# Kernel optimization log

Measured on AMD Instinct MI355X. Metric: run time of the kernel, lower is better.

## Reference

```python
import jax, jax.numpy as jnp
import numpy as np

BN_EPS = 1e-3  # Keras BatchNormalization default epsilon


def lstm_layer(x, h0, c0, W, U, b):
    # x: [B,T,D]; Keras gate order: i, f, g(cell), o
    def step(carry, xt):
        h, c = carry
        z = xt @ W + h @ U + b               # [B,4H]
        i, f, g, o = jnp.split(z, 4, axis=-1)
        c = jax.nn.sigmoid(f) * c + jax.nn.sigmoid(i) * jnp.tanh(g)
        h = jax.nn.sigmoid(o) * jnp.tanh(c)
        return (h, c), h
    (h, c), ys = jax.lax.scan(step, (h0, c0), x.transpose(1, 0, 2))
    return ys.transpose(1, 0, 2), h, c       # [B,T,H], [B,H], [B,H]


def setup_inputs() -> dict:
    key = jax.random.key(0)
    ks = jax.random.split(key, 8)
    B, T, V, D, H = 64, 128, 32000, 256, 1024
    s = 0.05
    return {
        "tokens": jax.random.randint(ks[0], (B, T), 0, V, dtype=jnp.int32),
        "h0": jnp.zeros((B, H), jnp.float32),
        "c0": jnp.zeros((B, H), jnp.float32),
        "emb": jax.random.normal(ks[1], (V, D), jnp.float32) * s,
        "W0": jax.random.normal(ks[2], (D, 4 * H), jnp.float32) * s,
        "U0": jax.random.normal(ks[3], (H, 4 * H), jnp.float32) * s,
        "b0": jnp.zeros((4 * H,), jnp.float32),
        "W1": jax.random.normal(ks[4], (H, 4 * H), jnp.float32) * s,
        "U1": jax.random.normal(ks[5], (H, 4 * H), jnp.float32) * s,
        "b1": jnp.zeros((4 * H,), jnp.float32),
        "gamma": jnp.ones((H,), jnp.float32),
        "beta": jnp.zeros((H,), jnp.float32),
        "mov_mean": jnp.zeros((H,), jnp.float32),
        "mov_var": jnp.ones((H,), jnp.float32),
    }


def reference(tokens, h0, c0, emb, W0, U0, b0, W1, U1, b1, gamma, beta, mov_mean, mov_var):
    x = emb[tokens]                                   # [B,T,D] embedding lookup
    # Original call() feeds the SAME `hidden` as initial state of layer 0,
    # then the (h,c) of layer 0 as initial state of layer 1 — replicate that.
    x, h, c = lstm_layer(x, h0, c0, W0, U0, b0)
    out, h, c = lstm_layer(x, h, c, W1, U1, b1)
    # BatchNormalization at inference (dropout inactive, moving stats used)
    inv = jax.lax.rsqrt(mov_var + BN_EPS)
    norm = (out - mov_mean) * inv * gamma + beta
    return norm, h, c
```

## Files before the change

### kernel.cpp

```cpp
#include <hip/hip_runtime.h>
#include <hip/hip_bf16.h>


typedef __attribute__((ext_vector_type(8))) short short8;
typedef __attribute__((ext_vector_type(4))) short short4v;
typedef __attribute__((ext_vector_type(4))) float f32x4;
typedef __attribute__((ext_vector_type(16))) float f32x16;
typedef unsigned short ushort_t;

__device__ __forceinline__ void lgkm0_bar() {
  asm volatile("s_waitcnt lgkmcnt(0)" ::: "memory");
  __builtin_amdgcn_s_barrier();
}

__device__ __forceinline__ ushort_t f2b(float f) {
  __hip_bfloat16 h = __float2bfloat16(f);
  return *reinterpret_cast<ushort_t*>(&h);
}
__device__ __forceinline__ float b2f(ushort_t u) {
  unsigned int x = ((unsigned int)u) << 16;
  return __builtin_bit_cast(float, x);
}
__device__ __forceinline__ float fsigmoid(float x) {
  return 1.f / (1.f + __expf(-x));
}
__device__ __forceinline__ float ftanh(float x) {
  return 1.f - 2.f / (__expf(2.f * x) + 1.f);
}

__device__ __forceinline__ void gload_lds16(const ushort_t* g, ushort_t* l) {
  __builtin_amdgcn_global_load_lds(
      (const __attribute__((address_space(1))) unsigned int*)g,
      (__attribute__((address_space(3))) unsigned int*)l, 16, 0, 0);
}

__device__ __forceinline__ size_t chunkoff(int b, int kcg, int NKS) {
  return (size_t)((((b >> 5) * NKS + (kcg >> 1)) << 6) |
                  ((b & 31) | ((kcg & 1) << 5))) * 8;
}

__global__ __launch_bounds__(256) void k_convert(
    const float* __restrict__ src, ushort_t* __restrict__ dst, int kshift) {
  size_t tid = (size_t)blockIdx.x * 256 + threadIdx.x;
  int k = (int)(tid >> 12);
  int c = (int)(tid & 4095);
  int pc = ((c & 1023) << 2) | (c >> 10);
  dst[((size_t)pc << kshift) + k] = f2b(src[tid]);
}

__global__ __launch_bounds__(256) void k_convert_ucoop(
    const float* __restrict__ src, ushort_t* __restrict__ dst) {
  int cid = blockIdx.x * 256 + threadIdx.x;
  int l = cid & 63;
  int ks = (cid >> 6) & 63;
  int nt = (cid >> 12) & 1;
  int w = cid >> 13;
  int pc = w * 64 + nt * 32 + (l & 31);
  int c = ((pc & 3) << 10) | (pc >> 2);
  int kb = ks * 16 + (l >> 5) * 8;
  short8 v;
#pragma unroll
  for (int e = 0; e < 8; ++e)
    v[e] = (short)f2b(src[(size_t)(kb + e) * 4096 + c]);
  *(short8*)(dst + (size_t)cid * 8) = v;
}

__global__ __launch_bounds__(256) void k_bias(
    const float* __restrict__ b0, const float* __restrict__ b1,
    float* __restrict__ bp0, float* __restrict__ bp1) {
  int pc = blockIdx.x * 256 + threadIdx.x;
  int c = ((pc & 3) << 10) | (pc >> 2);
  bp0[pc] = b0[c];
  bp1[pc] = b1[c];
}

__global__ __launch_bounds__(256) void k_gather(
    const int* __restrict__ tokens, const float* __restrict__ emb,
    ushort_t* __restrict__ Xef) {
  int row = blockIdx.x;
  int t = row >> 6, b = row & 63;
  int tok = tokens[b * 128 + t];
  int d = threadIdx.x;
  Xef[(size_t)t * 16384 + chunkoff(b, d >> 3, 16) + (d & 7)] =
      f2b(emb[(size_t)tok * 256 + d]);
}

__global__ __launch_bounds__(256) void k_init(
    const float* __restrict__ h0, const float* __restrict__ c0,
    ushort_t* __restrict__ hall, float* __restrict__ c_st,
    unsigned* __restrict__ bars) {
  int tid = blockIdx.x * 256 + threadIdx.x;
  int b = tid >> 10, jj = tid & 1023;
  c_st[tid] = c0[tid];
  hall[chunkoff(b, jj >> 3, 64) + (jj & 7)] = f2b(h0[tid]);
  if (tid < 2) bars[tid] = 0;
}

template <int NKS>
__global__ __launch_bounds__(256) void k_gemm(
    const ushort_t* __restrict__ Af, const ushort_t* __restrict__ BT,
    ushort_t* __restrict__ C) {
  const int K = NKS * 16;
  const int xcd = blockIdx.x & 7, loc = blockIdx.x >> 3;
  const int wgM = xcd * 8 + (loc & 7);
  const int wgN = loc >> 3;
  const int tid = threadIdx.x;
  const int l = tid & 63;
  const int wv = tid >> 6;
  const int wvM = wv & 1, wvN = wv >> 1;

  __shared__ __align__(16) ushort_t Alds[4096];
  __shared__ __align__(16) ushort_t Blds[4096];

  const int m0 = wgM * 128, n0 = wgN * 128;
  f32x4 acc[4][4] = {};

  for (int k0 = 0; k0 < K; k0 += 32) {
    __syncthreads();
#pragma unroll
    for (int jj = 0; jj < 2; ++jj) {
      int c = jj * 256 + tid;
      int kc = c >> 7, r = c & 127;
      int R = m0 + r, tt = R >> 6, b = R & 63;
      int kcg = (k0 >> 3) + kc;
      gload_lds16(Af + (size_t)tt * (NKS * 1024) + chunkoff(b, kcg, NKS),
                  (ushort_t*)&Alds[(size_t)(jj * 256 + (tid & ~63)) * 8]);
      gload_lds16(BT + (size_t)(n0 + r) * K + k0 + kc * 8,
                  (ushort_t*)&Blds[(size_t)(jj * 256 + (tid & ~63)) * 8]);
    }
    __syncthreads();

    short8 af[4], bf[4];
#pragma unroll
    for (int mt = 0; mt < 4; ++mt)
      af[mt] = *(const short8*)&Alds[((l >> 4) * 128 + wvM * 64 + mt * 16 + (l & 15)) * 8];
#pragma unroll
    for (int nt = 0; nt < 4; ++nt)
      bf[nt] = *(const short8*)&Blds[((l >> 4) * 128 + wvN * 64 + nt * 16 + (l & 15)) * 8];
#pragma unroll
    for (int mt = 0; mt < 4; ++mt)
#pragma unroll
      for (int nt = 0; nt < 4; ++nt)
        acc[mt][nt] =
            __builtin_amdgcn_mfma_f32_16x16x32_bf16(af[mt], bf[nt], acc[mt][nt], 0, 0, 0);
  }

  const int rr0 = wgM * 128 + wvM * 64 + (l >> 4) * 4;
  const int cc0 = wgN * 128 + wvN * 64 + (l & 15);
#pragma unroll
  for (int mt = 0; mt < 4; ++mt)
#pragma unroll
    for (int nt = 0; nt < 4; ++nt)
#pragma unroll
      for (int r = 0; r < 4; ++r)
        C[(size_t)(rr0 + mt * 16 + r) * 4096 + cc0 + nt * 16] =
            f2b(acc[mt][nt][r]);
}

template <int LAYER>
__global__ __launch_bounds__(256, 1) void k_pers(
    const ushort_t* __restrict__ Uf,
    const ushort_t* __restrict__ XW,
    const float* __restrict__ bp,
    ushort_t* __restrict__ hall,
    float* __restrict__ c_st,
    float* __restrict__ outp,
    const float* __restrict__ gamma, const float* __restrict__ beta,
    const float* __restrict__ mean, const float* __restrict__ var,
    unsigned* __restrict__ bar) {
  const int bid = blockIdx.x;
  const int w = bid >> 1;
  const int m = bid & 1;
  const int tid = threadIdx.x;
  const int l = tid & 63;
  const int wv = tid >> 6;
  const int nt = wv & 1, kh = wv >> 1;

  __shared__ __align__(16) ushort_t Ulds[2][64][512];
  __shared__ __align__(16) char smem[16896];
  __shared__ ushort_t hbuf[32][16];
  ushort_t(*stage)[512] = (ushort_t(*)[512])smem;
  float(*zls)[2][32][33] = (float(*)[2][32][33])smem;

  {
    const ushort_t* src = Uf + (size_t)w * 65536;
    for (int i = tid; i < 8192; i += 256)
      *(short8*)((ushort_t*)Ulds + (size_t)i * 8) =
          *(const short8*)(src + (size_t)i * 8);
  }

  const int jl = tid & 15, bq = tid >> 4;
  const int j = w * 16 + jl;
  float creg[2];
#pragma unroll
  for (int q = 0; q < 2; ++q)
    creg[q] = c_st[(m * 32 + bq * 2 + q) * 1024 + j];
  const f32x4 bias_v = *(const f32x4*)(bp + w * 64 + jl * 4);
  float scl = 0.f, sft = 0.f;
  if (LAYER == 1) {
    float inv = rsqrtf(var[j] + 1e-3f);
    scl = inv * gamma[j];
    sft = beta[j] - mean[j] * scl;
  }
  lgkm0_bar();

  for (int t = 0; t < 128; ++t) {
    const ushort_t* hin =
        hall + (size_t)((LAYER == 1 && t == 0) ? 128 : t) * 65536;
    ushort_t* hout = hall + (size_t)(t + 1) * 65536;

    short4v xw[2];
#pragma unroll
    for (int q = 0; q < 2; ++q)
      xw[q] = *(const short4v*)(
          XW + ((size_t)(t * 64 + m * 32 + bq * 2 + q) << 12) + w * 64 + jl * 4);

    short8 hr[4][4];
#pragma unroll
    for (int ph = 0; ph < 4; ++ph)
#pragma unroll
      for (int i = 0; i < 4; ++i) {
        int ks = ph * 16 + wv * 4 + i;
        hr[ph][i] = *(const short8*)(hin + (size_t)((m * 64 + ks) * 64 + l) * 8);
      }

    f32x16 acc[4] = {};
#pragma unroll
    for (int ph = 0; ph < 4; ++ph) {
      lgkm0_bar();
#pragma unroll
      for (int i = 0; i < 4; ++i)
        *(short8*)&stage[wv * 4 + i][l * 8] = hr[ph][i];
      lgkm0_bar();
#pragma unroll
      for (int i2 = 0; i2 < 8; ++i2) {
        int ksl = kh * 8 + i2;
        short8 a = *(const short8*)&stage[ksl][l * 8];
        short8 b = *(const short8*)&Ulds[nt][ph * 16 + ksl][l * 8];
        acc[i2 & 3] =
            __builtin_amdgcn_mfma_f32_32x32x16_bf16(a, b, acc[i2 & 3], 0, 0, 0);
      }
    }
    lgkm0_bar();

    f32x16 zt = acc[0] + acc[1] + acc[2] + acc[3];
#pragma unroll
    for (int r = 0; r < 16; ++r) {
      int row = (r & 3) + 8 * (r >> 2) + 4 * (l >> 5);
      zls[kh][nt][row][l & 31] = zt[r];
    }
    lgkm0_bar();

#pragma unroll
    for (int q = 0; q < 2; ++q) {
      const int b_loc = bq * 2 + q;
      const int nte = jl >> 3;
      const int cb = (jl & 7) * 4;
      float zi = zls[0][nte][b_loc][cb + 0] + zls[1][nte][b_loc][cb + 0] +
                 b2f((ushort_t)xw[q][0]) + bias_v[0];
      float zf = zls[0][nte][b_loc][cb + 1] + zls[1][nte][b_loc][cb + 1] +
                 b2f((ushort_t)xw[q][1]) + bias_v[1];
      float zg = zls[0][nte][b_loc][cb + 2] + zls[1][nte][b_loc][cb + 2] +
                 b2f((ushort_t)xw[q][2]) + bias_v[2];
      float zo = zls[0][nte][b_loc][cb + 3] + zls[1][nte][b_loc][cb + 3] +
                 b2f((ushort_t)xw[q][3]) + bias_v[3];
      float ii = fsigmoid(zi), ff = fsigmoid(zf), oo = fsigmoid(zo);
      float gg = ftanh(zg);
      creg[q] = ff * creg[q] + ii * gg;
      float hn = oo * ftanh(creg[q]);
      hbuf[b_loc][jl] = f2b(hn);
      const int b = m * 32 + b_loc;
      if (LAYER == 1) {
        outp[((size_t)b * 128 + t) * 1024 + j] = hn * scl + sft;
        if (t == 127) {
          outp[8388608 + b * 1024 + j] = hn;
          outp[8454144 + b * 1024 + j] = creg[q];
        }
      } else {
        if (t == 127) c_st[b * 1024 + j] = creg[q];
      }
    }
    lgkm0_bar();

    if (tid < 64) {
      short8 v = *(const short8*)&hbuf[l & 31][(l >> 5) * 8];
      union { short8 s; unsigned u[4]; } cv;
      cv.s = v;
      unsigned* dst = (unsigned*)(hout + (size_t)((m * 64 + w) * 64 + l) * 8);
#pragma unroll
      for (int wi = 0; wi < 4; ++wi)
        __hip_atomic_store(dst + wi, cv.u[wi], __ATOMIC_RELAXED,
                           __HIP_MEMORY_SCOPE_AGENT);
    }

    asm volatile("s_waitcnt vmcnt(0)" ::: "memory");
    __builtin_amdgcn_s_barrier();
    if (tid == 0) {
      __hip_atomic_fetch_add(bar, 1u, __ATOMIC_RELAXED,
                             __HIP_MEMORY_SCOPE_AGENT);
      unsigned tg = 128u * (unsigned)(t + 1);
      while (__hip_atomic_load(bar, __ATOMIC_RELAXED,
                               __HIP_MEMORY_SCOPE_AGENT) < tg)
        __builtin_amdgcn_s_sleep(8);
    }
    __builtin_amdgcn_s_barrier();
  }
}

extern "C" void kernel_launch(void* const* d_in, const int* in_sizes, int n_in,
                              void* d_out, int out_size, void* d_ws,
                              size_t ws_size, hipStream_t stream) {
  const int* tokens = (const int*)d_in[0];
  const float* h0 = (const float*)d_in[1];
  const float* c0 = (const float*)d_in[2];
  const float* emb = (const float*)d_in[3];
  const float* W0 = (const float*)d_in[4];
  const float* U0 = (const float*)d_in[5];
  const float* b0 = (const float*)d_in[6];
  const float* W1 = (const float*)d_in[7];
  const float* U1 = (const float*)d_in[8];
  const float* b1 = (const float*)d_in[9];
  const float* gammap = (const float*)d_in[10];
  const float* betap = (const float*)d_in[11];
  const float* mmean = (const float*)d_in[12];
  const float* mvar = (const float*)d_in[13];

  char* ws = (char*)d_ws;
  ushort_t* Uc0 = (ushort_t*)(ws + 0);
  ushort_t* Uc1 = (ushort_t*)(ws + 8388608);
  ushort_t* W0f = (ushort_t*)(ws + 16777216);
  ushort_t* W1f = (ushort_t*)(ws + 18874368);
  float* bp0 = (float*)(ws + 27262976);
  float* bp1 = (float*)(ws + 27279360);
  ushort_t* Xef = (ushort_t*)(ws + 27295744);
  ushort_t* XW = (ushort_t*)(ws + 31490048);
  ushort_t* hall = (ushort_t*)(ws + 98598912);
  float* c_st = (float*)(ws + 115507200);
  unsigned* bars = (unsigned*)(ws + 115769344);

  k_convert_ucoop<<<2048, 256, 0, stream>>>(U0, Uc0);
  k_convert_ucoop<<<2048, 256, 0, stream>>>(U1, Uc1);
  k_convert<<<4096, 256, 0, stream>>>(W0, W0f, 8);
  k_convert<<<16384, 256, 0, stream>>>(W1, W1f, 10);
  k_bias<<<16, 256, 0, stream>>>(b0, b1, bp0, bp1);
  k_gather<<<8192, 256, 0, stream>>>(tokens, emb, Xef);
  k_init<<<256, 256, 0, stream>>>(h0, c0, hall, c_st, bars);

  float* outp = (float*)d_out;

  k_gemm<16><<<2048, 256, 0, stream>>>(Xef, W0f, XW);
  k_pers<0><<<128, 256, 0, stream>>>(Uc0, XW, bp0, hall, c_st, nullptr,
                                     nullptr, nullptr, nullptr, nullptr,
                                     bars + 0);

  k_gemm<64><<<2048, 256, 0, stream>>>(hall + 65536, W1f, XW);
  k_pers<1><<<128, 256, 0, stream>>>(Uc1, XW, bp1, hall, c_st, outp, gammap,
                                     betap, mmean, mvar, bars + 1);
}
```

Before: 1.553 ms.

## Halve persistent LSTM blocks, load h directly to registers with software prefetch

The persistent recurrent kernel now runs 64 blocks instead of 128, with each block covering all 64 batch rows for its 16 hidden units. Each wave owns a full M-tile and N-tile, so the K-split reduction across waves and the LDS staging of h go away. The h fragments are read straight from global memory through a triple-buffered prefetch pipeline, and the grid barrier spin sleep is shortened. Fewer blocks means fewer participants in the per-step grid barrier and fewer LDS barriers per step, at the cost of more work per block and higher register pressure.

```diff
diff --git a/kernel.cpp b/kernel.cpp
--- a/kernel.cpp
+++ b/kernel.cpp
@@ -168,19 +168,15 @@
     const float* __restrict__ gamma, const float* __restrict__ beta,
     const float* __restrict__ mean, const float* __restrict__ var,
     unsigned* __restrict__ bar) {
-  const int bid = blockIdx.x;
-  const int w = bid >> 1;
-  const int m = bid & 1;
+  const int w = blockIdx.x;
   const int tid = threadIdx.x;
   const int l = tid & 63;
   const int wv = tid >> 6;
-  const int nt = wv & 1, kh = wv >> 1;
+  const int mt = wv & 1, nt = wv >> 1;
 
   __shared__ __align__(16) ushort_t Ulds[2][64][512];
-  __shared__ __align__(16) char smem[16896];
-  __shared__ ushort_t hbuf[32][16];
-  ushort_t(*stage)[512] = (ushort_t(*)[512])smem;
-  float(*zls)[2][32][33] = (float(*)[2][32][33])smem;
+  __shared__ float zls[4][32][33];
+  __shared__ ushort_t hbuf[64][16];
 
   {
     const ushort_t* src = Uf + (size_t)w * 65536;
@@ -191,10 +187,10 @@
 
   const int jl = tid & 15, bq = tid >> 4;
   const int j = w * 16 + jl;
-  float creg[2];
-#pragma unroll
-  for (int q = 0; q < 2; ++q)
-    creg[q] = c_st[(m * 32 + bq * 2 + q) * 1024 + j];
+  float creg[4];
+#pragma unroll
+  for (int q = 0; q < 4; ++q)
+    creg[q] = c_st[(bq + q * 16) * 1024 + j];
   const f32x4 bias_v = *(const f32x4*)(bp + w * 64 + jl * 4);
   float scl = 0.f, sft = 0.f;
   if (LAYER == 1) {
@@ -204,72 +200,69 @@
   }
   lgkm0_bar();
 
+#pragma unroll 1
   for (int t = 0; t < 128; ++t) {
     const ushort_t* hin =
         hall + (size_t)((LAYER == 1 && t == 0) ? 128 : t) * 65536;
     ushort_t* hout = hall + (size_t)(t + 1) * 65536;
 
-    short4v xw[2];
-#pragma unroll
-    for (int q = 0; q < 2; ++q)
+    short4v xw[4];
+#pragma unroll
+    for (int q = 0; q < 4; ++q)
       xw[q] = *(const short4v*)(
-          XW + ((size_t)(t * 64 + m * 32 + bq * 2 + q) << 12) + w * 64 + jl * 4);
-
-    short8 hr[4][4];
-#pragma unroll
-    for (int ph = 0; ph < 4; ++ph)
-#pragma unroll
-      for (int i = 0; i < 4; ++i) {
-        int ks = ph * 16 + wv * 4 + i;
-        hr[ph][i] = *(const short8*)(hin + (size_t)((m * 64 + ks) * 64 + l) * 8);
+          XW + ((size_t)(t * 64 + bq + q * 16) << 12) + w * 64 + jl * 4);
+
+    const ushort_t* Ab = hin + (size_t)mt * 32768 + (size_t)l * 8;
+    f32x16 acc[4] = {};
+    short8 gA[8], gB[8], gC[8];
+    auto pf8 = [&](short8(&dst)[8], int ks) {
+#pragma unroll
+      for (int i = 0; i < 8; ++i)
+        dst[i] = *(const short8*)(Ab + (size_t)(ks + i) * 512);
+    };
+    auto mma8 = [&](short8(&cur)[8], int ks) {
+#pragma unroll
+      for (int i = 0; i < 8; ++i) {
+        short8 bfr = *(const short8*)&Ulds[nt][ks + i][l * 8];
+        acc[i & 3] = __builtin_amdgcn_mfma_f32_32x32x16_bf16(cur[i], bfr,
+                                                             acc[i & 3], 0, 0, 0);
       }
-
-    f32x16 acc[4] = {};
-#pragma unroll
-    for (int ph = 0; ph < 4; ++ph) {
-      lgkm0_bar();
-#pragma unroll
-      for (int i = 0; i < 4; ++i)
-        *(short8*)&stage[wv * 4 + i][l * 8] = hr[ph][i];
-      lgkm0_bar();
-#pragma unroll
-      for (int i2 = 0; i2 < 8; ++i2) {
-        int ksl = kh * 8 + i2;
-        short8 a = *(const short8*)&stage[ksl][l * 8];
-        short8 b = *(const short8*)&Ulds[nt][ph * 16 + ksl][l * 8];
-        acc[i2 & 3] =
-            __builtin_amdgcn_mfma_f32_32x32x16_bf16(a, b, acc[i2 & 3], 0, 0, 0);
-      }
-    }
-    lgkm0_bar();
+    };
+    pf8(gA, 0);
+    pf8(gB, 8);
+    pf8(gC, 16); mma8(gA, 0);
+    pf8(gA, 24); mma8(gB, 8);
+    pf8(gB, 32); mma8(gC, 16);
+    pf8(gC, 40); mma8(gA, 24);
+    pf8(gA, 48); mma8(gB, 32);
+    pf8(gB, 56); mma8(gC, 40);
+    mma8(gA, 48);
+    mma8(gB, 56);
 
     f32x16 zt = acc[0] + acc[1] + acc[2] + acc[3];
 #pragma unroll
     for (int r = 0; r < 16; ++r) {
       int row = (r & 3) + 8 * (r >> 2) + 4 * (l >> 5);
-      zls[kh][nt][row][l & 31] = zt[r];
+      zls[wv][row][l & 31] = zt[r];
     }
     lgkm0_bar();
 
 #pragma unroll
-    for (int q = 0; q < 2; ++q) {
-      const int b_loc = bq * 2 + q;
-      const int nte = jl >> 3;
+    for (int q = 0; q < 4; ++q) {
+      const int b = bq + q * 16;
+      const int wve = (jl >> 3) * 2 + (q >> 1);
+      const int rowe = bq + (q & 1) * 16;
       const int cb = (jl & 7) * 4;
-      float zi = zls[0][nte][b_loc][cb + 0] + zls[1][nte][b_loc][cb + 0] +
-                 b2f((ushort_t)xw[q][0]) + bias_v[0];
-      float zf = zls[0][nte][b_loc][cb + 1] + zls[1][nte][b_loc][cb + 1] +
-                 b2f((ushort_t)xw[q][1]) + bias_v[1];
-      float zg = zls[0][nte][b_loc][cb + 2] + zls[1][nte][b_loc][cb + 2] +
-                 b2f((ushort_t)xw[q][2]) + bias_v[2];
-      float zo = zls[0][nte][b_loc][cb + 3] + zls[1][nte][b_loc][cb + 3] +
-                 b2f((ushort_t)xw[q][3]) + bias_v[3];
+      f32x4 zv = *(const f32x4*)&zls[wve][rowe][cb];
+      float zi = zv[0] + b2f((ushort_t)xw[q][0]) + bias_v[0];
+      float zf = zv[1] + b2f((ushort_t)xw[q][1]) + bias_v[1];
+      float zg = zv[2] + b2f((ushort_t)xw[q][2]) + bias_v[2];
+      float zo = zv[3] + b2f((ushort_t)xw[q][3]) + bias_v[3];
       float ii = fsigmoid(zi), ff = fsigmoid(zf), oo = fsigmoid(zo);
       float gg = ftanh(zg);
       creg[q] = ff * creg[q] + ii * gg;
       float hn = oo * ftanh(creg[q]);
-      hbuf[b_loc][jl] = f2b(hn);
-      const int b = m * 32 + b_loc;
+      hbuf[b][jl] = f2b(hn);
       if (LAYER == 1) {
         outp[((size_t)b * 128 + t) * 1024 + j] = hn * scl + sft;
         if (t == 127) {
@@ -282,11 +275,13 @@
     }
     lgkm0_bar();
 
-    if (tid < 64) {
-      short8 v = *(const short8*)&hbuf[l & 31][(l >> 5) * 8];
+    if (tid < 128) {
+      const int rb = tid >> 6, l2 = tid & 63;
+      const int brow = rb * 32 + (l2 & 31);
+      short8 v = *(const short8*)&hbuf[brow][(l2 >> 5) * 8];
       union { short8 s; unsigned u[4]; } cv;
       cv.s = v;
-      unsigned* dst = (unsigned*)(hout + (size_t)((m * 64 + w) * 64 + l) * 8);
+      unsigned* dst = (unsigned*)(hout + (size_t)((rb * 64 + w) * 64 + l2) * 8);
 #pragma unroll
       for (int wi = 0; wi < 4; ++wi)
         __hip_atomic_store(dst + wi, cv.u[wi], __ATOMIC_RELAXED,
@@ -298,10 +293,10 @@
     if (tid == 0) {
       __hip_atomic_fetch_add(bar, 1u, __ATOMIC_RELAXED,
                              __HIP_MEMORY_SCOPE_AGENT);
-      unsigned tg = 128u * (unsigned)(t + 1);
+      unsigned tg = 64u * (unsigned)(t + 1);
       while (__hip_atomic_load(bar, __ATOMIC_RELAXED,
                                __HIP_MEMORY_SCOPE_AGENT) < tg)
-        __builtin_amdgcn_s_sleep(8);
+        __builtin_amdgcn_s_sleep(2);
     }
     __builtin_amdgcn_s_barrier();
   }
@@ -349,11 +344,11 @@
   float* outp = (float*)d_out;
 
   k_gemm<16><<<2048, 256, 0, stream>>>(Xef, W0f, XW);
-  k_pers<0><<<128, 256, 0, stream>>>(Uc0, XW, bp0, hall, c_st, nullptr,
-                                     nullptr, nullptr, nullptr, nullptr,
-                                     bars + 0);
+  k_pers<0><<<64, 256, 0, stream>>>(Uc0, XW, bp0, hall, c_st, nullptr,
+                                    nullptr, nullptr, nullptr, nullptr,
+                                    bars + 0);
 
   k_gemm<64><<<2048, 256, 0, stream>>>(hall + 65536, W1f, XW);
-  k_pers<1><<<128, 256, 0, stream>>>(Uc1, XW, bp1, hall, c_st, outp, gammap,
-                                     betap, mmean, mvar, bars + 1);
-}
+  k_pers<1><<<64, 256, 0, stream>>>(Uc1, XW, bp1, hall, c_st, outp, gammap,
+                                    betap, mmean, mvar, bars + 1);
+}
```

New measurement: 2.803 ms. 1.8x slower.
